# Optimization experiments

Hardware: AMD Instinct MI355X
Metric: run time of the kernel (lower is better)

The kernel has to match this reference:

```python
import jax, jax.numpy as jnp
import numpy as np

B, L, D, H, O = 512, 256, 256, 128, 256  # batch, max_len, input_dim, hidden_dim, output_dim


def setup_inputs() -> dict:
    key = jax.random.key(0)
    ks = jax.random.split(key, 16)
    s = 0.1
    n = jax.random.normal
    return {
        "sequences": n(ks[0], (B, L, D), jnp.float32),
        "seqlens": jax.random.randint(ks[1], (B,), 1, L + 1, jnp.int32),
        # forward-direction GRU params (PyTorch layout: gates [r, z, n] stacked)
        "Wih_f": s * n(ks[2], (3 * H, D), jnp.float32),
        "Whh_f": s * n(ks[3], (3 * H, H), jnp.float32),
        "bih_f": s * n(ks[4], (3 * H,), jnp.float32),
        "bhh_f": s * n(ks[5], (3 * H,), jnp.float32),
        # backward-direction GRU params
        "Wih_b": s * n(ks[6], (3 * H, D), jnp.float32),
        "Whh_b": s * n(ks[7], (3 * H, H), jnp.float32),
        "bih_b": s * n(ks[8], (3 * H,), jnp.float32),
        "bhh_b": s * n(ks[9], (3 * H,), jnp.float32),
        # attention MLP + context vector
        "W_mlp": s * n(ks[10], (O, 2 * H), jnp.float32),
        "b_mlp": s * n(ks[11], (O,), jnp.float32),
        "ctx": s * n(ks[12], (O,), jnp.float32),
    }


def _gru(xs, mask, Wih, Whh, bih, bhh, reverse):
    """Masked GRU scan. xs: [L,B,D], mask: [L,B,1]. Returns hidden states [L,B,H]."""
    def step(h, inp):
        x_t, m_t = inp
        gx = x_t @ Wih.T + bih          # [B, 3H]
        gh = h @ Whh.T + bhh            # [B, 3H]
        xr, xz, xn = jnp.split(gx, 3, axis=-1)
        hr, hz, hn = jnp.split(gh, 3, axis=-1)
        r = jax.nn.sigmoid(xr + hr)
        z = jax.nn.sigmoid(xz + hz)
        cand = jnp.tanh(xn + r * hn)
        h_new = (1.0 - z) * cand + z * h
        h = jnp.where(m_t, h_new, h)    # hold state on padding steps
        return h, h

    h0 = jnp.zeros((xs.shape[1], Whh.shape[1]), xs.dtype)
    _, hs = jax.lax.scan(step, h0, (xs, mask), reverse=reverse)
    return hs


def reference(sequences, seqlens, Wih_f, Whh_f, bih_f, bhh_f, Wih_b, Whh_b, bih_b, bhh_b, W_mlp, b_mlp, ctx):
    mask = jnp.arange(L)[None, :] < seqlens[:, None]      # [B, L] valid-token mask
    xs = sequences.transpose(1, 0, 2)                      # [L, B, D]
    m = mask.T[:, :, None]                                 # [L, B, 1]
    hf = _gru(xs, m, Wih_f, Whh_f, bih_f, bhh_f, False)    # forward direction
    hb = _gru(xs, m, Wih_b, Whh_b, bih_b, bhh_b, True)     # backward direction
    rnn_out = jnp.concatenate([hf, hb], axis=-1).transpose(1, 0, 2)  # [B, L, 2H]
    mlp_out = jnp.tanh(rnn_out @ W_mlp.T + b_mlp)          # [B, L, O]
    scores = jnp.einsum('blo,o->bl', mlp_out, ctx)         # [B, L]
    neg = jnp.finfo(scores.dtype).min
    w = jax.nn.softmax(jnp.where(mask, scores, neg), axis=1)  # per-sequence softmax over valid positions
    return jnp.einsum('bl,blh->bh', w, rnn_out)            # [B, 2H] attention-pooled embedding
```

## Files before the change

kernel.cpp:

```cpp
#include <hip/hip_runtime.h>
#include <hip/hip_bf16.h>
#include <cstdint>
#include <cstddef>

#define BATCH 512
#define SEQL 256
#define DIN 256
#define HID 128
#define OUTD 256
#define G3 384
#define TCH 64
#define NCH 4
#define NBS 16
#define NGRPS (BATCH/NBS)
#define MTOT (BATCH*SEQL)
#define MCH  (BATCH*TCH)
#define HSPAD 136
#define NGXT 3072

typedef __attribute__((ext_vector_type(8))) short short8v;
typedef __attribute__((ext_vector_type(4))) float float4v;

__device__ __forceinline__ unsigned short f2bf_u(float x) {
  union { float f; uint32_t u; } v; v.f = x;
  uint32_t r = v.u + 0x7FFFu + ((v.u >> 16) & 1u);
  return (unsigned short)(r >> 16);
}
__device__ __forceinline__ float bfu2f(unsigned short u) {
  union { uint32_t u; float f; } v; v.u = ((uint32_t)u) << 16; return v.f;
}
__device__ __forceinline__ float fast_tanh(float x) {
  float e2 = __expf(-2.0f * x);
  return (1.0f - e2) / (1.0f + e2);
}

__global__ __launch_bounds__(256) void prep_split(
    const float* __restrict__ Wm, unsigned short* __restrict__ mhi, unsigned short* __restrict__ mlo,
    const float* __restrict__ Wf, unsigned short* __restrict__ fhi, unsigned short* __restrict__ flo,
    const float* __restrict__ Wb, unsigned short* __restrict__ bhi, unsigned short* __restrict__ blo)
{
  int gid = blockIdx.x * 256 + threadIdx.x;
  const float* src; unsigned short* hi; unsigned short* lo; int off;
  if (gid < 16384)      { src = Wm; hi = mhi; lo = mlo; off = gid * 4; }
  else if (gid < 40960) { src = Wf; hi = fhi; lo = flo; off = (gid - 16384) * 4; }
  else                  { src = Wb; hi = bhi; lo = blo; off = (gid - 40960) * 4; }
  float4 w4 = *(const float4*)&src[off];
  ushort4 h4, l4;
  h4.x = f2bf_u(w4.x); l4.x = f2bf_u(w4.x - bfu2f(h4.x));
  h4.y = f2bf_u(w4.y); l4.y = f2bf_u(w4.y - bfu2f(h4.y));
  h4.z = f2bf_u(w4.z); l4.z = f2bf_u(w4.z - bfu2f(h4.z));
  h4.w = f2bf_u(w4.w); l4.w = f2bf_u(w4.w - bfu2f(h4.w));
  *(ushort4*)&hi[off] = h4;
  *(ushort4*)&lo[off] = l4;
}

__device__ __forceinline__ void gx_tile(
    int tid, int m0, int yy,
    const float* __restrict__ X,
    const unsigned short* __restrict__ WhiF, const unsigned short* __restrict__ WloF,
    const unsigned short* __restrict__ WhiB, const unsigned short* __restrict__ WloB,
    const float* __restrict__ bf, const float* __restrict__ bb,
    unsigned short* __restrict__ bufF, unsigned short* __restrict__ bufB, int cF, int cB,
    unsigned short* Abf, unsigned short* Bhi, unsigned short* Blo)
{
  const unsigned short* Whi; const unsigned short* Wlo;
  const float* bias; unsigned short* buf; int c;
  if (yy < 6) { Whi = WhiF; Wlo = WloF; bias = bf; buf = bufF; c = cF; }
  else        { yy -= 6; Whi = WhiB; Wlo = WloB; bias = bb; buf = bufB; c = cB; }
  const int n0 = yy * 64;

  const int l  = tid & 63;
  const int w  = tid >> 6;
  const int fr = l & 15;
  const int fk = (l >> 4) * 8;

  float4v acc[2][4];
#pragma unroll
  for (int a = 0; a < 2; ++a)
#pragma unroll
    for (int nb = 0; nb < 4; ++nb) acc[a][nb] = (float4v)0.0f;

  for (int k0 = 0; k0 < DIN; k0 += 32) {
#pragma unroll
    for (int j = 0; j < 4; ++j) {
      int row = (tid >> 3) + j * 32;
      int kq  = (tid & 7) * 4;
      int r   = m0 + row;
      int b_  = r >> 6, tt = r & 63;
      int xrow = b_ * SEQL + c * TCH + tt;
      float4 x4 = *(const float4*)&X[(size_t)xrow * DIN + k0 + kq];
      ushort4 h4 = {f2bf_u(x4.x), f2bf_u(x4.y), f2bf_u(x4.z), f2bf_u(x4.w)};
      *(ushort4*)&Abf[row * 40 + kq] = h4;
    }
    {
      int half = tid & 1;
      int cc   = tid >> 1;
      int col  = cc >> 1;
      int seg  = (cc & 1) * 16;
      const unsigned short* srcw = (half ? Wlo : Whi) + (size_t)(n0 + col) * DIN + k0 + seg;
      unsigned short* dst = (half ? Blo : Bhi) + col * 40 + seg;
      *(short8v*)dst       = *(const short8v*)srcw;
      *(short8v*)(dst + 8) = *(const short8v*)(srcw + 8);
    }
    __syncthreads();

    short8v ah[2], bh[4], blv[4];
#pragma unroll
    for (int a = 0; a < 2; ++a)
      ah[a] = *(const short8v*)&Abf[(w * 32 + a * 16 + fr) * 40 + fk];
#pragma unroll
    for (int nb = 0; nb < 4; ++nb) {
      bh[nb]  = *(const short8v*)&Bhi[(nb * 16 + fr) * 40 + fk];
      blv[nb] = *(const short8v*)&Blo[(nb * 16 + fr) * 40 + fk];
    }
#pragma unroll
    for (int a = 0; a < 2; ++a)
#pragma unroll
      for (int nb = 0; nb < 4; ++nb) {
        acc[a][nb] = __builtin_amdgcn_mfma_f32_16x16x32_bf16(ah[a], bh[nb],  acc[a][nb], 0, 0, 0);
        acc[a][nb] = __builtin_amdgcn_mfma_f32_16x16x32_bf16(ah[a], blv[nb], acc[a][nb], 0, 0, 0);
      }
    __syncthreads();
  }

#pragma unroll
  for (int a = 0; a < 2; ++a)
#pragma unroll
    for (int nb = 0; nb < 4; ++nb) {
      int gate = n0 + nb * 16 + fr;
      float bv_ = bias[gate];
#pragma unroll
      for (int reg = 0; reg < 4; ++reg) {
        int r = m0 + w * 32 + a * 16 + (l >> 4) * 4 + reg;
        buf[(size_t)r * G3 + gate] = f2bf_u(acc[a][nb][reg] + bv_);
      }
    }
}

template<int P>
__device__ __forceinline__ void gru_step(
    unsigned short (*hsbuf)[NBS * HSPAD], int col, int rq, int hidx,
    const short8v (&Bh)[3][4], const short8v (&Bl)[3][4], const float (&bias_)[3],
    const float (&G)[3][4], float (&hold)[4], const int (&len_)[4], int t,
    __hip_bfloat16* (&rp)[4], int drp)
{
  const unsigned short* rd = &hsbuf[P][col * HSPAD + rq * 8];
  short8v ah[4];
#pragma unroll
  for (int ks = 0; ks < 4; ++ks)
    ah[ks] = *(const short8v*)(rd + ks * 32);

  float4v a0 = (float4v){bias_[0] + G[0][0], bias_[0] + G[0][1], bias_[0] + G[0][2], bias_[0] + G[0][3]};
  float4v a1 = (float4v){bias_[1] + G[1][0], bias_[1] + G[1][1], bias_[1] + G[1][2], bias_[1] + G[1][3]};
  float4v a2 = (float4v){bias_[2], bias_[2], bias_[2], bias_[2]};
  float4v l0 = (float4v)0.0f, l1 = (float4v)0.0f, l2 = (float4v)0.0f;
#pragma unroll
  for (int ks = 0; ks < 4; ++ks) {
    a0 = __builtin_amdgcn_mfma_f32_16x16x32_bf16(ah[ks], Bh[0][ks], a0, 0, 0, 0);
    l0 = __builtin_amdgcn_mfma_f32_16x16x32_bf16(ah[ks], Bl[0][ks], l0, 0, 0, 0);
    a1 = __builtin_amdgcn_mfma_f32_16x16x32_bf16(ah[ks], Bh[1][ks], a1, 0, 0, 0);
    l1 = __builtin_amdgcn_mfma_f32_16x16x32_bf16(ah[ks], Bl[1][ks], l1, 0, 0, 0);
    a2 = __builtin_amdgcn_mfma_f32_16x16x32_bf16(ah[ks], Bh[2][ks], a2, 0, 0, 0);
    l2 = __builtin_amdgcn_mfma_f32_16x16x32_bf16(ah[ks], Bl[2][ks], l2, 0, 0, 0);
  }
  a0 += l0; a1 += l1; a2 += l2;

  unsigned short* wr = &hsbuf[P ^ 1][rq * 4 * HSPAD + hidx];
#pragma unroll
  for (int reg = 0; reg < 4; ++reg) {
    float gr = a0[reg], gz = a1[reg], gn = a2[reg], xn = G[2][reg];
    float r = 1.0f / (1.0f + __expf(-gr));
    float z = 1.0f / (1.0f + __expf(-gz));
    float e2 = __expf(-2.0f * (xn + r * gn));
    float cand = (1.0f - e2) / (1.0f + e2);
    float hv = cand + z * (hold[reg] - cand);
    bool act = (t < len_[reg]);
    hv = act ? hv : hold[reg];
    hold[reg] = hv;
    wr[reg * HSPAD] = f2bf_u(hv);
    if (act) *rp[reg] = __float2bfloat16(hv);
    rp[reg] += drp;
  }
  asm volatile("s_waitcnt lgkmcnt(0)" ::: "memory");
  __builtin_amdgcn_s_barrier();
  __builtin_amdgcn_sched_barrier(0);
}

__device__ __forceinline__ void scan_block(
    int sb, int tid,
    const int* __restrict__ seqlens,
    const float* __restrict__ Whh_f, const float* __restrict__ Whh_b,
    const float* __restrict__ bhh_f, const float* __restrict__ bhh_b,
    const unsigned short* __restrict__ bufF, const unsigned short* __restrict__ bufB,
    float* __restrict__ hstate, __hip_bfloat16* __restrict__ rnn, int ci,
    unsigned short (*hsbuf)[NBS * HSPAD])
{
  const int fwd = (sb < NGRPS) ? 1 : 0;
  const int grp = fwd ? sb : (sb - NGRPS);
  const int b0  = grp * NBS;
  const int w   = tid >> 6;
  const int l   = tid & 63;
  const int col = l & 15;
  const int rq  = l >> 4;
  const int hidx = w * 16 + col;
  const float* Whh = fwd ? Whh_f : Whh_b;
  const float* bhh = fwd ? bhh_f : bhh_b;
  const unsigned short* buf = fwd ? bufF : bufB;
  const int c = fwd ? ci : (NCH - 1 - ci);

  __builtin_amdgcn_s_setprio(1);

  short8v Bh[3][4], Bl[3][4];
  float bias_[3];
#pragma unroll
  for (int j = 0; j < 3; ++j) {
    const int g = j * HID + hidx;
    bias_[j] = bhh[g];
#pragma unroll
    for (int ks = 0; ks < 4; ++ks) {
      const float* p = Whh + (size_t)g * HID + ks * 32 + rq * 8;
      float4 x0 = *(const float4*)p;
      float4 x1 = *(const float4*)(p + 4);
      float v[8] = {x0.x, x0.y, x0.z, x0.w, x1.x, x1.y, x1.z, x1.w};
      short8v hi8, lo8;
#pragma unroll
      for (int e = 0; e < 8; ++e) {
        unsigned short h = f2bf_u(v[e]);
        hi8[e] = (short)h;
        lo8[e] = (short)f2bf_u(v[e] - bfu2f(h));
      }
      Bh[j][ks] = hi8; Bl[j][ks] = lo8;
    }
  }

  int len_[4];
#pragma unroll
  for (int reg = 0; reg < 4; ++reg) len_[reg] = seqlens[b0 + rq * 4 + reg];
  int gmax = 0;
  for (int nb = 0; nb < NBS; ++nb) gmax = max(gmax, seqlens[b0 + nb]);

  float* hst = hstate + ((size_t)((fwd ? 0 : 1) * NGRPS + grp)) * (NBS * HID);
  float hold[4];
#pragma unroll
  for (int reg = 0; reg < 4; ++reg) {
    int nb = rq * 4 + reg;
    hold[reg] = (ci == 0) ? 0.0f : hst[nb * HID + hidx];
    hsbuf[0][nb * HSPAD + hidx] = f2bf_u(hold[reg]);
  }
  __syncthreads();

  int nsteps = gmax - c * TCH;
  nsteps = (nsteps > TCH) ? TCH : nsteps;

  const int tcb  = c * TCH;
  const int dofs = fwd ? 0 : HID;

  if (nsteps == TCH) {
    const int tt0 = fwd ? 0 : (TCH - 1);
    const int dt  = fwd ? 1 : -1;
    const int dgp = fwd ? G3 : -G3;
    const int drp = fwd ? OUTD : -OUTD;

    const unsigned short* gp[4];
    __hip_bfloat16* rp[4];
#pragma unroll
    for (int reg = 0; reg < 4; ++reg) {
      gp[reg] = buf + (size_t)((b0 + rq * 4 + reg) * TCH + tt0) * G3 + hidx;
      rp[reg] = rnn + (size_t)((b0 + rq * 4 + reg) * SEQL + tcb + tt0) * OUTD + dofs + hidx;
    }

    float GA[3][4], GB[3][4];
    auto LOADGX = [&](float (&G)[3][4]) {
#pragma unroll
      for (int reg = 0; reg < 4; ++reg) {
        G[0][reg] = bfu2f(gp[reg][0]);
        G[1][reg] = bfu2f(gp[reg][HID]);
        G[2][reg] = bfu2f(gp[reg][2 * HID]);
        gp[reg] += dgp;
      }
    };
    LOADGX(GA);
    LOADGX(GB);

    int t = tcb + tt0;
#pragma unroll 1
    for (int it = 0; it < TCH / 2; ++it) {
      gru_step<0>(hsbuf, col, rq, hidx, Bh, Bl, bias_, GA, hold, len_, t, rp, drp);
      t += dt;
      LOADGX(GA);
      gru_step<1>(hsbuf, col, rq, hidx, Bh, Bl, bias_, GB, hold, len_, t, rp, drp);
      t += dt;
      LOADGX(GB);
    }
  } else if (nsteps > 0) {
    float gxc[3][4], gxn[3][4];
    {
      int tt0 = fwd ? 0 : (nsteps - 1);
#pragma unroll
      for (int j = 0; j < 3; ++j)
#pragma unroll
        for (int reg = 0; reg < 4; ++reg)
          gxc[j][reg] = bfu2f(buf[(size_t)((b0 + rq * 4 + reg) * TCH + tt0) * G3 + j * HID + hidx]);
    }

    int cur = 0;
    for (int ss = 0; ss < nsteps; ++ss) {
      const int tt = fwd ? ss : (nsteps - 1 - ss);
      const int t  = tcb + tt;

      short8v ah[4];
#pragma unroll
      for (int ks = 0; ks < 4; ++ks)
        ah[ks] = *(const short8v*)&hsbuf[cur][col * HSPAD + ks * 32 + rq * 8];

      {
        int ssn = (ss + 1 < nsteps) ? (ss + 1) : ss;
        int ttn = fwd ? ssn : (nsteps - 1 - ssn);
#pragma unroll
        for (int j = 0; j < 3; ++j)
#pragma unroll
          for (int reg = 0; reg < 4; ++reg)
            gxn[j][reg] = bfu2f(buf[(size_t)((b0 + rq * 4 + reg) * TCH + ttn) * G3 + j * HID + hidx]);
      }

      float4v acc[3], accl[3];
#pragma unroll
      for (int j = 0; j < 3; ++j) {
        acc[j]  = (float4v){bias_[j], bias_[j], bias_[j], bias_[j]};
        accl[j] = (float4v)0.0f;
      }
#pragma unroll
      for (int ks = 0; ks < 4; ++ks) {
#pragma unroll
        for (int j = 0; j < 3; ++j) {
          acc[j]  = __builtin_amdgcn_mfma_f32_16x16x32_bf16(ah[ks], Bh[j][ks], acc[j],  0, 0, 0);
          accl[j] = __builtin_amdgcn_mfma_f32_16x16x32_bf16(ah[ks], Bl[j][ks], accl[j], 0, 0, 0);
        }
      }
#pragma unroll
      for (int j = 0; j < 3; ++j) acc[j] += accl[j];

#pragma unroll
      for (int reg = 0; reg < 4; ++reg) {
        int nb = rq * 4 + reg;
        float gr = acc[0][reg] + gxc[0][reg];
        float gz = acc[1][reg] + gxc[1][reg];
        float gn = acc[2][reg];
        float xn = gxc[2][reg];
        float r = 1.0f / (1.0f + __expf(-gr));
        float z = 1.0f / (1.0f + __expf(-gz));
        float e2 = __expf(-2.0f * (xn + r * gn));
        float cand = (1.0f - e2) / (1.0f + e2);
        float hv = (1.0f - z) * cand + z * hold[reg];
        bool act = (t < len_[reg]);
        hv = act ? hv : hold[reg];
        hold[reg] = hv;
        hsbuf[cur ^ 1][nb * HSPAD + hidx] = f2bf_u(hv);
        if (act)
          rnn[(size_t)((b0 + nb) * SEQL + t) * OUTD + dofs + hidx] = __float2bfloat16(hv);
      }
      asm volatile("s_waitcnt lgkmcnt(0)" ::: "memory");
      __builtin_amdgcn_s_barrier();
      __builtin_amdgcn_sched_barrier(0);
      cur ^= 1;

#pragma unroll
      for (int j = 0; j < 3; ++j)
#pragma unroll
        for (int reg = 0; reg < 4; ++reg) gxc[j][reg] = gxn[j][reg];
    }
  }

  __builtin_amdgcn_s_setprio(0);

#pragma unroll
  for (int reg = 0; reg < 4; ++reg)
    hst[(rq * 4 + reg) * HID + hidx] = hold[reg];
}

__device__ __forceinline__ void mlp64_tile(
    int tid, int m0, int nh,
    const __hip_bfloat16* __restrict__ rnn,
    const unsigned short* __restrict__ Whi, const unsigned short* __restrict__ Wlo,
    const float* __restrict__ bmlp, const float* __restrict__ ctx,
    float* __restrict__ scoresH,
    unsigned short* Abf, unsigned short* BhiS, unsigned short* BloS)
{
  const int l  = tid & 63;
  const int w  = tid >> 6;
  const int fr = l & 15;
  const int fk = (l >> 4) * 8;

  float bl_[8], cl_[8];
#pragma unroll
  for (int nt = 0; nt < 8; ++nt) {
    bl_[nt] = bmlp[nh * 128 + nt * 16 + fr];
    cl_[nt] = ctx[nh * 128 + nt * 16 + fr];
  }

  float4v acc[8];
#pragma unroll
  for (int nt = 0; nt < 8; ++nt) acc[nt] = (float4v)0.0f;

  for (int k0 = 0; k0 < OUTD; k0 += 32) {
    {
      int row = tid >> 2;
      int kq  = (tid & 3) * 8;
      *(short8v*)&Abf[row * 40 + kq] =
          *(const short8v*)((const short*)rnn + (size_t)(m0 + row) * OUTD + k0 + kq);
    }
#pragma unroll
    for (int j = 0; j < 2; ++j) {
      int cid  = tid * 2 + j;
      int half = cid >> 8;
      int cc   = cid & 255;
      int colx = cc >> 1;
      int seg  = (cc & 1) * 16;
      const unsigned short* srcw = (half ? Wlo : Whi) + (size_t)(nh * 128 + colx) * OUTD + k0 + seg;
      unsigned short* dst = (half ? BloS : BhiS) + colx * 40 + seg;
      *(short8v*)dst       = *(const short8v*)srcw;
      *(short8v*)(dst + 8) = *(const short8v*)(srcw + 8);
    }
    __syncthreads();

    short8v a = *(const short8v*)&Abf[(w * 16 + fr) * 40 + fk];
#pragma unroll
    for (int nt = 0; nt < 8; ++nt) {
      short8v bh = *(const short8v*)&BhiS[(nt * 16 + fr) * 40 + fk];
      short8v bv = *(const short8v*)&BloS[(nt * 16 + fr) * 40 + fk];
      acc[nt] = __builtin_amdgcn_mfma_f32_16x16x32_bf16(a, bh, acc[nt], 0, 0, 0);
      acc[nt] = __builtin_amdgcn_mfma_f32_16x16x32_bf16(a, bv, acc[nt], 0, 0, 0);
    }
    __syncthreads();
  }

  float p[4] = {0.f, 0.f, 0.f, 0.f};
#pragma unroll
  for (int nt = 0; nt < 8; ++nt) {
    float bv_ = bl_[nt], cv = cl_[nt];
#pragma unroll
    for (int reg = 0; reg < 4; ++reg)
      p[reg] += fast_tanh(acc[nt][reg] + bv_) * cv;
  }
#pragma unroll
  for (int off = 1; off < 16; off <<= 1)
#pragma unroll
    for (int reg = 0; reg < 4; ++reg) p[reg] += __shfl_xor(p[reg], off, 64);
  if (fr == 0) {
#pragma unroll
    for (int reg = 0; reg < 4; ++reg)
      scoresH[(size_t)nh * MTOT + m0 + w * 16 + (l >> 4) * 4 + reg] = p[reg];
  }
}

__global__ __launch_bounds__(256) void gx_kernel(
    const float* __restrict__ X,
    const unsigned short* __restrict__ WhiF, const unsigned short* __restrict__ WloF,
    const unsigned short* __restrict__ WhiB, const unsigned short* __restrict__ WloB,
    const float* __restrict__ bf, const float* __restrict__ bb,
    unsigned short* __restrict__ bufF, unsigned short* __restrict__ bufB, int cF, int cB)
{
  __shared__ unsigned short Abf[128 * 40];
  __shared__ unsigned short Bhi[64 * 40];
  __shared__ unsigned short Blo[64 * 40];
  gx_tile(threadIdx.x, blockIdx.x * 128, blockIdx.y, X, WhiF, WloF, WhiB, WloB,
          bf, bb, bufF, bufB, cF, cB, Abf, Bhi, Blo);
}

__global__ __launch_bounds__(512, 2) void scan_kernel(
    const int* __restrict__ seqlens,
    const float* __restrict__ Whh_f, const float* __restrict__ Whh_b,
    const float* __restrict__ bhh_f, const float* __restrict__ bhh_b,
    const unsigned short* __restrict__ bufF, const unsigned short* __restrict__ bufB,
    float* __restrict__ hstate, __hip_bfloat16* __restrict__ rnn, int ci)
{
  __shared__ unsigned short hsbuf[2][NBS * HSPAD];
  scan_block(blockIdx.x, threadIdx.x, seqlens, Whh_f, Whh_b, bhh_f, bhh_b,
             bufF, bufB, hstate, rnn, ci, hsbuf);
}

__global__ __launch_bounds__(512, 2) void fused_kernel(
    const int* __restrict__ seqlens,
    const float* __restrict__ Whh_f, const float* __restrict__ Whh_b,
    const float* __restrict__ bhh_f, const float* __restrict__ bhh_b,
    const float* __restrict__ X,
    const unsigned short* __restrict__ WhiF, const unsigned short* __restrict__ WloF,
    const unsigned short* __restrict__ WhiB, const unsigned short* __restrict__ WloB,
    const float* __restrict__ bf, const float* __restrict__ bb,
    const unsigned short* __restrict__ rdF, const unsigned short* __restrict__ rdB,
    unsigned short* __restrict__ wrF, unsigned short* __restrict__ wrB,
    float* __restrict__ hstate, __hip_bfloat16* __restrict__ rnn, int ci)
{
  __shared__ unsigned short hsbuf[2][NBS * HSPAD];
  __shared__ unsigned short AbfS[2][128 * 40];
  __shared__ unsigned short BhiS[2][64 * 40];
  __shared__ unsigned short BloS[2][64 * 40];

  if (blockIdx.x < 2 * NGRPS) {
    scan_block(blockIdx.x, threadIdx.x, seqlens, Whh_f, Whh_b, bhh_f, bhh_b,
               rdF, rdB, hstate, rnn, ci, hsbuf);
  } else {
    const int gb   = blockIdx.x - 2 * NGRPS;
    const int half = threadIdx.x >> 8;
    const int htid = threadIdx.x & 255;
    const int t0   = gb * 2 + half;
    const int m0   = (t0 & 255) * 128;
    const int yy   = t0 >> 8;
    gx_tile(htid, m0, yy, X, WhiF, WloF, WhiB, WloB, bf, bb,
            wrF, wrB, ci + 1, NCH - 2 - ci, AbfS[half], BhiS[half], BloS[half]);
  }
}

union ShFinal {
  unsigned short hs[2][NBS * HSPAD];
  struct { unsigned short A[2][64 * 40]; unsigned short Bh[2][128 * 40]; unsigned short Bl[2][128 * 40]; } m;
};
__global__ __launch_bounds__(512, 2) void fused_final(
    const int* __restrict__ seqlens,
    const float* __restrict__ Whh_f, const float* __restrict__ Whh_b,
    const float* __restrict__ bhh_f, const float* __restrict__ bhh_b,
    const unsigned short* __restrict__ rdF, const unsigned short* __restrict__ rdB,
    float* __restrict__ hstate, __hip_bfloat16* __restrict__ rnn,
    const unsigned short* __restrict__ mhi, const unsigned short* __restrict__ mlo,
    const float* __restrict__ bmlp, const float* __restrict__ ctx,
    float* __restrict__ scoresH)
{
  __shared__ ShFinal sh;
  if (blockIdx.x < 2 * NGRPS) {
    scan_block(blockIdx.x, threadIdx.x, seqlens, Whh_f, Whh_b, bhh_f, bhh_b,
               rdF, rdB, hstate, rnn, NCH - 1, sh.hs);
  } else {
    const int gb   = blockIdx.x - 2 * NGRPS;
    const int half = threadIdx.x >> 8;
    const int htid = threadIdx.x & 255;
    const int body = gb * 2 + half;
    const int nh   = body & 1;
    const int tile = body >> 1;
    const int b    = tile >> 1;
    const int t0   = 64 + (tile & 1) * 64;
    const int m0   = b * SEQL + t0;
    mlp64_tile(htid, m0, nh, rnn, mhi, mlo, bmlp, ctx, scoresH,
               sh.m.A[half], sh.m.Bh[half], sh.m.Bl[half]);
  }
}

__global__ __launch_bounds__(256) void mlp_score(
    const __hip_bfloat16* __restrict__ rnn,
    const unsigned short* __restrict__ Whi, const unsigned short* __restrict__ Wlo,
    const float* __restrict__ bmlp, const float* __restrict__ ctx,
    float* __restrict__ scoresH)
{
  __shared__ unsigned short Abf[128 * 40];
  __shared__ unsigned short BhiS[128 * 40];
  __shared__ unsigned short BloS[128 * 40];

  const int tid = threadIdx.x;
  const int m0  = blockIdx.x * 128;
  const int nh  = blockIdx.y;
  const int l   = tid & 63;
  const int w   = tid >> 6;
  const int fr  = l & 15;
  const int fk  = (l >> 4) * 8;

  float bl_[8], cl_[8];
#pragma unroll
  for (int nt = 0; nt < 8; ++nt) {
    bl_[nt] = bmlp[nh * 128 + nt * 16 + fr];
    cl_[nt] = ctx[nh * 128 + nt * 16 + fr];
  }

  float4v acc[2][8];
#pragma unroll
  for (int a = 0; a < 2; ++a)
#pragma unroll
    for (int nt = 0; nt < 8; ++nt) acc[a][nt] = (float4v)0.0f;

  for (int k0 = 0; k0 < OUTD; k0 += 32) {
    {
      int row = tid >> 1;
      int kq  = (tid & 1) * 16;
      const short* src = (const short*)rnn + (size_t)(m0 + row) * OUTD + k0 + kq;
      *(short8v*)&Abf[row * 40 + kq]     = *(const short8v*)src;
      *(short8v*)&Abf[row * 40 + kq + 8] = *(const short8v*)(src + 8);
    }
#pragma unroll
    for (int j = 0; j < 2; ++j) {
      int cid  = tid * 2 + j;
      int half = cid >> 8;
      int cc   = cid & 255;
      int colx = cc >> 1;
      int seg  = (cc & 1) * 16;
      const unsigned short* srcw = (half ? Wlo : Whi) + (size_t)(nh * 128 + colx) * OUTD + k0 + seg;
      unsigned short* dst = (half ? BloS : BhiS) + colx * 40 + seg;
      *(short8v*)dst       = *(const short8v*)srcw;
      *(short8v*)(dst + 8) = *(const short8v*)(srcw + 8);
    }
    __syncthreads();

    short8v ah0 = *(const short8v*)&Abf[(w * 32 + fr) * 40 + fk];
    short8v ah1 = *(const short8v*)&Abf[(w * 32 + 16 + fr) * 40 + fk];
#pragma unroll
    for (int nt = 0; nt < 8; ++nt) {
      short8v bh = *(const short8v*)&BhiS[(nt * 16 + fr) * 40 + fk];
      short8v bv = *(const short8v*)&BloS[(nt * 16 + fr) * 40 + fk];
      acc[0][nt] = __builtin_amdgcn_mfma_f32_16x16x32_bf16(ah0, bh, acc[0][nt], 0, 0, 0);
      acc[0][nt] = __builtin_amdgcn_mfma_f32_16x16x32_bf16(ah0, bv, acc[0][nt], 0, 0, 0);
      acc[1][nt] = __builtin_amdgcn_mfma_f32_16x16x32_bf16(ah1, bh, acc[1][nt], 0, 0, 0);
      acc[1][nt] = __builtin_amdgcn_mfma_f32_16x16x32_bf16(ah1, bv, acc[1][nt], 0, 0, 0);
    }
    __syncthreads();
  }

#pragma unroll
  for (int a = 0; a < 2; ++a) {
    float p[4] = {0.f, 0.f, 0.f, 0.f};
#pragma unroll
    for (int nt = 0; nt < 8; ++nt) {
      float bv_ = bl_[nt], cv = cl_[nt];
#pragma unroll
      for (int reg = 0; reg < 4; ++reg)
        p[reg] += fast_tanh(acc[a][nt][reg] + bv_) * cv;
    }
#pragma unroll
    for (int off = 1; off < 16; off <<= 1)
#pragma unroll
      for (int reg = 0; reg < 4; ++reg) p[reg] += __shfl_xor(p[reg], off, 64);
    if (fr == 0) {
#pragma unroll
      for (int reg = 0; reg < 4; ++reg)
        scoresH[(size_t)nh * MTOT + m0 + w * 32 + a * 16 + (l >> 4) * 4 + reg] = p[reg];
    }
  }
}

__global__ __launch_bounds__(256) void mlp_score_rest(
    const __hip_bfloat16* __restrict__ rnn,
    const unsigned short* __restrict__ Whi, const unsigned short* __restrict__ Wlo,
    const float* __restrict__ bmlp, const float* __restrict__ ctx,
    float* __restrict__ scoresH)
{
  __shared__ unsigned short Abf[128 * 40];
  __shared__ unsigned short BhiS[128 * 40];
  __shared__ unsigned short BloS[128 * 40];

  const int tid = threadIdx.x;
  const int b   = blockIdx.x;
  const int nh  = blockIdx.y;
  const int l   = tid & 63;
  const int w   = tid >> 6;
  const int fr  = l & 15;
  const int fk  = (l >> 4) * 8;

  float bl_[8], cl_[8];
#pragma unroll
  for (int nt = 0; nt < 8; ++nt) {
    bl_[nt] = bmlp[nh * 128 + nt * 16 + fr];
    cl_[nt] = ctx[nh * 128 + nt * 16 + fr];
  }

  float4v acc[2][8];
#pragma unroll
  for (int a = 0; a < 2; ++a)
#pragma unroll
    for (int nt = 0; nt < 8; ++nt) acc[a][nt] = (float4v)0.0f;

  for (int k0 = 0; k0 < OUTD; k0 += 32) {
    {
      int row = tid >> 1;
      int kq  = (tid & 1) * 16;
      int t   = (row < 64) ? row : (row + 128);
      const short* src = (const short*)rnn + (size_t)(b * SEQL + t) * OUTD + k0 + kq;
      *(short8v*)&Abf[row * 40 + kq]     = *(const short8v*)src;
      *(short8v*)&Abf[row * 40 + kq + 8] = *(const short8v*)(src + 8);
    }
#pragma unroll
    for (int j = 0; j < 2; ++j) {
      int cid  = tid * 2 + j;
      int half = cid >> 8;
      int cc   = cid & 255;
      int colx = cc >> 1;
      int seg  = (cc & 1) * 16;
      const unsigned short* srcw = (half ? Wlo : Whi) + (size_t)(nh * 128 + colx) * OUTD + k0 + seg;
      unsigned short* dst = (half ? BloS : BhiS) + colx * 40 + seg;
      *(short8v*)dst       = *(const short8v*)srcw;
      *(short8v*)(dst + 8) = *(const short8v*)(srcw + 8);
    }
    __syncthreads();

    short8v ah0 = *(const short8v*)&Abf[(w * 32 + fr) * 40 + fk];
    short8v ah1 = *(const short8v*)&Abf[(w * 32 + 16 + fr) * 40 + fk];
#pragma unroll
    for (int nt = 0; nt < 8; ++nt) {
      short8v bh = *(const short8v*)&BhiS[(nt * 16 + fr) * 40 + fk];
      short8v bv = *(const short8v*)&BloS[(nt * 16 + fr) * 40 + fk];
      acc[0][nt] = __builtin_amdgcn_mfma_f32_16x16x32_bf16(ah0, bh, acc[0][nt], 0, 0, 0);
      acc[0][nt] = __builtin_amdgcn_mfma_f32_16x16x32_bf16(ah0, bv, acc[0][nt], 0, 0, 0);
      acc[1][nt] = __builtin_amdgcn_mfma_f32_16x16x32_bf16(ah1, bh, acc[1][nt], 0, 0, 0);
      acc[1][nt] = __builtin_amdgcn_mfma_f32_16x16x32_bf16(ah1, bv, acc[1][nt], 0, 0, 0);
    }
    __syncthreads();
  }

#pragma unroll
  for (int a = 0; a < 2; ++a) {
    float p[4] = {0.f, 0.f, 0.f, 0.f};
#pragma unroll
    for (int nt = 0; nt < 8; ++nt) {
      float bv_ = bl_[nt], cv = cl_[nt];
#pragma unroll
      for (int reg = 0; reg < 4; ++reg)
        p[reg] += fast_tanh(acc[a][nt][reg] + bv_) * cv;
    }
#pragma unroll
    for (int off = 1; off < 16; off <<= 1)
#pragma unroll
      for (int reg = 0; reg < 4; ++reg) p[reg] += __shfl_xor(p[reg], off, 64);
    if (fr == 0) {
#pragma unroll
      for (int reg = 0; reg < 4; ++reg) {
        int rr = w * 32 + a * 16 + (l >> 4) * 4 + reg;
        int t  = (rr < 64) ? rr : (rr + 128);
        scoresH[(size_t)nh * MTOT + b * SEQL + t] = p[reg];
      }
    }
  }
}

__global__ __launch_bounds__(256) void softmax_pool(
    const int* __restrict__ seqlens,
    const float* __restrict__ scoresH,
    const __hip_bfloat16* __restrict__ rnn,
    float* __restrict__ out)
{
  const int b = blockIdx.x;
  const int len = seqlens[b];
  const int tid = threadIdx.x;
  __shared__ float sm[SEQL];
  __shared__ float red[8];

  float s = (tid < len)
      ? (scoresH[b * SEQL + tid] + scoresH[(size_t)MTOT + b * SEQL + tid])
      : -3.4e38f;
  float wm = s;
#pragma unroll
  for (int off = 32; off > 0; off >>= 1) wm = fmaxf(wm, __shfl_xor(wm, off, 64));
  if ((tid & 63) == 0) red[tid >> 6] = wm;
  __syncthreads();
  float bm = fmaxf(fmaxf(red[0], red[1]), fmaxf(red[2], red[3]));

  float e = (tid < len) ? expf(s - bm) : 0.0f;
  sm[tid] = e;
  float sum = e;
#pragma unroll
  for (int off = 32; off > 0; off >>= 1) sum += __shfl_xor(sum, off, 64);
  if ((tid & 63) == 0) red[4 + (tid >> 6)] = sum;
  __syncthreads();
  float inv = 1.0f / (red[4] + red[5] + red[6] + red[7]);

  float acc = 0.0f;
  for (int l = 0; l < len; ++l)
    acc += sm[l] * __bfloat162float(rnn[(size_t)(b * SEQL + l) * OUTD + tid]);
  out[b * OUTD + tid] = acc * inv;
}

extern "C" void kernel_launch(void* const* d_in, const int* in_sizes, int n_in,
                              void* d_out, int out_size, void* d_ws, size_t ws_size,
                              hipStream_t stream) {
  const float* seq    = (const float*)d_in[0];
  const int*   lens   = (const int*)d_in[1];
  const float* Wih_f  = (const float*)d_in[2];
  const float* Whh_f  = (const float*)d_in[3];
  const float* bih_f  = (const float*)d_in[4];
  const float* bhh_f  = (const float*)d_in[5];
  const float* Wih_b  = (const float*)d_in[6];
  const float* Whh_b  = (const float*)d_in[7];
  const float* bih_b  = (const float*)d_in[8];
  const float* bhh_b  = (const float*)d_in[9];
  const float* Wmlp   = (const float*)d_in[10];
  const float* bmlp   = (const float*)d_in[11];
  const float* ctx    = (const float*)d_in[12];
  float* out = (float*)d_out;

  const size_t BUFSZ = (size_t)MCH * G3;
  const size_t needOverlap =
      4 * BUFSZ * 2 + (size_t)MTOT * OUTD * 2 + 2 * (size_t)MTOT * 4 +
      2 * BATCH * HID * 4 + 2 * (size_t)OUTD * OUTD * 2 + 4 * (size_t)G3 * DIN * 2;
  const bool overlap = (ws_size >= needOverlap);

  unsigned short* buf0F = (unsigned short*)d_ws;
  unsigned short* buf0B = buf0F + BUFSZ;
  unsigned short* buf1F = overlap ? (buf0B + BUFSZ) : buf0F;
  unsigned short* buf1B = overlap ? (buf1F + BUFSZ) : buf0B;
  unsigned short* tail  = overlap ? (buf1B + BUFSZ) : (buf0B + BUFSZ);

  __hip_bfloat16* rnn  = (__hip_bfloat16*)tail;
  float* scoresH = (float*)((unsigned short*)rnn + (size_t)MTOT * OUTD);
  float* hstate  = scoresH + 2 * (size_t)MTOT;
  unsigned short* mhi = (unsigned short*)(hstate + 2 * BATCH * HID);
  unsigned short* mlo = mhi + OUTD * OUTD;
  unsigned short* fhi = mlo + OUTD * OUTD;
  unsigned short* flo = fhi + G3 * DIN;
  unsigned short* bhi2 = flo + G3 * DIN;
  unsigned short* blo2 = bhi2 + G3 * DIN;

  prep_split<<<dim3(256), 256, 0, stream>>>(Wmlp, mhi, mlo, Wih_f, fhi, flo, Wih_b, bhi2, blo2);

  if (overlap) {
    unsigned short* bp[2][2] = {{buf0F, buf0B}, {buf1F, buf1B}};
    gx_kernel<<<dim3(256, 12), 256, 0, stream>>>(seq, fhi, flo, bhi2, blo2, bih_f, bih_b,
                                                 bp[0][0], bp[0][1], 0, NCH - 1);
    for (int k = 0; k < NCH - 1; ++k) {
      fused_kernel<<<dim3(2 * NGRPS + NGXT / 2), 512, 0, stream>>>(
          lens, Whh_f, Whh_b, bhh_f, bhh_b,
          seq, fhi, flo, bhi2, blo2, bih_f, bih_b,
          bp[k & 1][0], bp[k & 1][1], bp[(k + 1) & 1][0], bp[(k + 1) & 1][1],
          hstate, rnn, k);
    }
    fused_final<<<dim3(2 * NGRPS + 1024), 512, 0, stream>>>(
        lens, Whh_f, Whh_b, bhh_f, bhh_b,
        bp[(NCH - 1) & 1][0], bp[(NCH - 1) & 1][1], hstate, rnn,
        mhi, mlo, bmlp, ctx, scoresH);
    mlp_score_rest<<<dim3(512, 2), 256, 0, stream>>>(rnn, mhi, mlo, bmlp, ctx, scoresH);
  } else {
    for (int ci = 0; ci < NCH; ++ci) {
      gx_kernel<<<dim3(256, 12), 256, 0, stream>>>(seq, fhi, flo, bhi2, blo2, bih_f, bih_b,
                                                   buf0F, buf0B, ci, NCH - 1 - ci);
      scan_kernel<<<dim3(2 * NGRPS), 512, 0, stream>>>(
          lens, Whh_f, Whh_b, bhh_f, bhh_b, buf0F, buf0B, hstate, rnn, ci);
    }
    mlp_score<<<dim3(MTOT / 128, 2), 256, 0, stream>>>(rnn, mhi, mlo, bmlp, ctx, scoresH);
  }

  softmax_pool<<<dim3(BATCH), 256, 0, stream>>>(lens, scoresH, rnn, out);
}
```

Before: 525.3 us.

## Fuse remaining MLP scoring with softmax pooling and deepen gx prefetch in scan

The separate mlp_score_rest and softmax_pool launches are merged into one per-batch tail_kernel. It computes the MLP scores for the remaining timesteps of both output halves, combines them with the precomputed middle scores in shared memory, and then does the masked softmax and pooling. This removes one launch and the global round-trip of those scores, but halves the grid from 1024 to 512 blocks. The GRU scan loop also now prefetches the input-gate values two steps ahead as raw bf16 in a 4-deep rotation, to hide global load latency behind the recurrent step.

Result: slower. 627.1 us (+19.4%).

```diff
diff --git a/kernel.cpp b/kernel.cpp
--- a/kernel.cpp
+++ b/kernel.cpp
@@ -34,6 +34,8 @@
   return (1.0f - e2) / (1.0f + e2);
 }
 
+struct GxB { unsigned short v[3][4]; };
+
 __global__ __launch_bounds__(256) void prep_split(
     const float* __restrict__ Wm, unsigned short* __restrict__ mhi, unsigned short* __restrict__ mlo,
     const float* __restrict__ Wf, unsigned short* __restrict__ fhi, unsigned short* __restrict__ flo,
@@ -138,20 +140,32 @@
 }
 
 template<int P>
-__device__ __forceinline__ void gru_step(
+__device__ __forceinline__ void gru_step2(
     unsigned short (*hsbuf)[NBS * HSPAD], int col, int rq, int hidx,
     const short8v (&Bh)[3][4], const short8v (&Bl)[3][4], const float (&bias_)[3],
-    const float (&G)[3][4], float (&hold)[4], const int (&len_)[4], int t,
+    const GxB& Gc, GxB& Gl,
+    const unsigned short* (&gp)[4], int dgp,
+    float (&hold)[4], const int (&len_)[4], int t,
     __hip_bfloat16* (&rp)[4], int drp)
 {
+#pragma unroll
+  for (int reg = 0; reg < 4; ++reg) {
+    Gl.v[0][reg] = gp[reg][0];
+    Gl.v[1][reg] = gp[reg][HID];
+    Gl.v[2][reg] = gp[reg][2 * HID];
+    gp[reg] += dgp;
+  }
+
   const unsigned short* rd = &hsbuf[P][col * HSPAD + rq * 8];
   short8v ah[4];
 #pragma unroll
   for (int ks = 0; ks < 4; ++ks)
     ah[ks] = *(const short8v*)(rd + ks * 32);
 
-  float4v a0 = (float4v){bias_[0] + G[0][0], bias_[0] + G[0][1], bias_[0] + G[0][2], bias_[0] + G[0][3]};
-  float4v a1 = (float4v){bias_[1] + G[1][0], bias_[1] + G[1][1], bias_[1] + G[1][2], bias_[1] + G[1][3]};
+  float4v a0 = (float4v){bias_[0] + bfu2f(Gc.v[0][0]), bias_[0] + bfu2f(Gc.v[0][1]),
+                         bias_[0] + bfu2f(Gc.v[0][2]), bias_[0] + bfu2f(Gc.v[0][3])};
+  float4v a1 = (float4v){bias_[1] + bfu2f(Gc.v[1][0]), bias_[1] + bfu2f(Gc.v[1][1]),
+                         bias_[1] + bfu2f(Gc.v[1][2]), bias_[1] + bfu2f(Gc.v[1][3])};
   float4v a2 = (float4v){bias_[2], bias_[2], bias_[2], bias_[2]};
   float4v l0 = (float4v)0.0f, l1 = (float4v)0.0f, l2 = (float4v)0.0f;
 #pragma unroll
@@ -168,7 +182,8 @@
   unsigned short* wr = &hsbuf[P ^ 1][rq * 4 * HSPAD + hidx];
 #pragma unroll
   for (int reg = 0; reg < 4; ++reg) {
-    float gr = a0[reg], gz = a1[reg], gn = a2[reg], xn = G[2][reg];
+    float gr = a0[reg], gz = a1[reg], gn = a2[reg];
+    float xn = bfu2f(Gc.v[2][reg]);
     float r = 1.0f / (1.0f + __expf(-gr));
     float z = 1.0f / (1.0f + __expf(-gz));
     float e2 = __expf(-2.0f * (xn + r * gn));
@@ -269,28 +284,25 @@
       rp[reg] = rnn + (size_t)((b0 + rq * 4 + reg) * SEQL + tcb + tt0) * OUTD + dofs + hidx;
     }
 
-    float GA[3][4], GB[3][4];
-    auto LOADGX = [&](float (&G)[3][4]) {
-#pragma unroll
-      for (int reg = 0; reg < 4; ++reg) {
-        G[0][reg] = bfu2f(gp[reg][0]);
-        G[1][reg] = bfu2f(gp[reg][HID]);
-        G[2][reg] = bfu2f(gp[reg][2 * HID]);
-        gp[reg] += dgp;
-      }
-    };
-    LOADGX(GA);
-    LOADGX(GB);
+    GxB g0, g1, g2, g3;
+#pragma unroll
+    for (int reg = 0; reg < 4; ++reg) {
+      g0.v[0][reg] = gp[reg][0]; g0.v[1][reg] = gp[reg][HID]; g0.v[2][reg] = gp[reg][2 * HID];
+      gp[reg] += dgp;
+    }
+#pragma unroll
+    for (int reg = 0; reg < 4; ++reg) {
+      g1.v[0][reg] = gp[reg][0]; g1.v[1][reg] = gp[reg][HID]; g1.v[2][reg] = gp[reg][2 * HID];
+      gp[reg] += dgp;
+    }
 
     int t = tcb + tt0;
 #pragma unroll 1
-    for (int it = 0; it < TCH / 2; ++it) {
-      gru_step<0>(hsbuf, col, rq, hidx, Bh, Bl, bias_, GA, hold, len_, t, rp, drp);
-      t += dt;
-      LOADGX(GA);
-      gru_step<1>(hsbuf, col, rq, hidx, Bh, Bl, bias_, GB, hold, len_, t, rp, drp);
-      t += dt;
-      LOADGX(GB);
+    for (int it = 0; it < TCH / 4; ++it) {
+      gru_step2<0>(hsbuf, col, rq, hidx, Bh, Bl, bias_, g0, g2, gp, dgp, hold, len_, t, rp, drp); t += dt;
+      gru_step2<1>(hsbuf, col, rq, hidx, Bh, Bl, bias_, g1, g3, gp, dgp, hold, len_, t, rp, drp); t += dt;
+      gru_step2<0>(hsbuf, col, rq, hidx, Bh, Bl, bias_, g2, g0, gp, dgp, hold, len_, t, rp, drp); t += dt;
+      gru_step2<1>(hsbuf, col, rq, hidx, Bh, Bl, bias_, g3, g1, gp, dgp, hold, len_, t, rp, drp); t += dt;
     }
   } else if (nsteps > 0) {
     float gxc[3][4], gxn[3][4];
@@ -544,6 +556,137 @@
   }
 }
 
+__global__ __launch_bounds__(256) void tail_kernel(
+    const int* __restrict__ seqlens,
+    const __hip_bfloat16* __restrict__ rnn,
+    const unsigned short* __restrict__ Whi, const unsigned short* __restrict__ Wlo,
+    const float* __restrict__ bmlp, const float* __restrict__ ctx,
+    const float* __restrict__ scoresH,
+    float* __restrict__ out)
+{
+  __shared__ unsigned short Abf[128 * 40];
+  __shared__ unsigned short BhiS[128 * 40];
+  __shared__ unsigned short BloS[128 * 40];
+  __shared__ float sm[SEQL];
+  __shared__ float red[8];
+
+  const int tid = threadIdx.x;
+  const int b   = blockIdx.x;
+  const int len = seqlens[b];
+  const int l   = tid & 63;
+  const int w   = tid >> 6;
+  const int fr  = l & 15;
+  const int fk  = (l >> 4) * 8;
+
+  float pfull[2][4] = {{0.f, 0.f, 0.f, 0.f}, {0.f, 0.f, 0.f, 0.f}};
+
+  for (int nh = 0; nh < 2; ++nh) {
+    float bl_[8], cl_[8];
+#pragma unroll
+    for (int nt = 0; nt < 8; ++nt) {
+      bl_[nt] = bmlp[nh * 128 + nt * 16 + fr];
+      cl_[nt] = ctx[nh * 128 + nt * 16 + fr];
+    }
+
+    float4v acc[2][8];
+#pragma unroll
+    for (int a = 0; a < 2; ++a)
+#pragma unroll
+      for (int nt = 0; nt < 8; ++nt) acc[a][nt] = (float4v)0.0f;
+
+    for (int k0 = 0; k0 < OUTD; k0 += 32) {
+      {
+        int row = tid >> 1;
+        int kq  = (tid & 1) * 16;
+        int t   = (row < 64) ? row : (row + 128);
+        const short* src = (const short*)rnn + (size_t)(b * SEQL + t) * OUTD + k0 + kq;
+        *(short8v*)&Abf[row * 40 + kq]     = *(const short8v*)src;
+        *(short8v*)&Abf[row * 40 + kq + 8] = *(const short8v*)(src + 8);
+      }
+#pragma unroll
+      for (int j = 0; j < 2; ++j) {
+        int cid  = tid * 2 + j;
+        int half = cid >> 8;
+        int cc   = cid & 255;
+        int colx = cc >> 1;
+        int seg  = (cc & 1) * 16;
+        const unsigned short* srcw = (half ? Wlo : Whi) + (size_t)(nh * 128 + colx) * OUTD + k0 + seg;
+        unsigned short* dst = (half ? BloS : BhiS) + colx * 40 + seg;
+        *(short8v*)dst       = *(const short8v*)srcw;
+        *(short8v*)(dst + 8) = *(const short8v*)(srcw + 8);
+      }
+      __syncthreads();
+
+      short8v ah0 = *(const short8v*)&Abf[(w * 32 + fr) * 40 + fk];
+      short8v ah1 = *(const short8v*)&Abf[(w * 32 + 16 + fr) * 40 + fk];
+#pragma unroll
+      for (int nt = 0; nt < 8; ++nt) {
+        short8v bh = *(const short8v*)&BhiS[(nt * 16 + fr) * 40 + fk];
+        short8v bv = *(const short8v*)&BloS[(nt * 16 + fr) * 40 + fk];
+        acc[0][nt] = __builtin_amdgcn_mfma_f32_16x16x32_bf16(ah0, bh, acc[0][nt], 0, 0, 0);
+        acc[0][nt] = __builtin_amdgcn_mfma_f32_16x16x32_bf16(ah0, bv, acc[0][nt], 0, 0, 0);
+        acc[1][nt] = __builtin_amdgcn_mfma_f32_16x16x32_bf16(ah1, bh, acc[1][nt], 0, 0, 0);
+        acc[1][nt] = __builtin_amdgcn_mfma_f32_16x16x32_bf16(ah1, bv, acc[1][nt], 0, 0, 0);
+      }
+      __syncthreads();
+    }
+
+#pragma unroll
+    for (int a = 0; a < 2; ++a)
+#pragma unroll
+      for (int nt = 0; nt < 8; ++nt) {
+        float bv_ = bl_[nt], cv = cl_[nt];
+#pragma unroll
+        for (int reg = 0; reg < 4; ++reg)
+          pfull[a][reg] += fast_tanh(acc[a][nt][reg] + bv_) * cv;
+      }
+  }
+
+#pragma unroll
+  for (int a = 0; a < 2; ++a) {
+#pragma unroll
+    for (int off = 1; off < 16; off <<= 1)
+#pragma unroll
+      for (int reg = 0; reg < 4; ++reg) pfull[a][reg] += __shfl_xor(pfull[a][reg], off, 64);
+  }
+  if (fr == 0) {
+#pragma unroll
+    for (int a = 0; a < 2; ++a)
+#pragma unroll
+      for (int reg = 0; reg < 4; ++reg) {
+        int rr = w * 32 + a * 16 + (l >> 4) * 4 + reg;
+        int t  = (rr < 64) ? rr : (rr + 128);
+        sm[t] = pfull[a][reg];
+      }
+  }
+  if (tid < 128)
+    sm[64 + tid] = scoresH[b * SEQL + 64 + tid] + scoresH[(size_t)MTOT + b * SEQL + 64 + tid];
+  __syncthreads();
+
+  float s = (tid < len) ? sm[tid] : -3.4e38f;
+  float wm = s;
+#pragma unroll
+  for (int off = 32; off > 0; off >>= 1) wm = fmaxf(wm, __shfl_xor(wm, off, 64));
+  if ((tid & 63) == 0) red[tid >> 6] = wm;
+  __syncthreads();
+  float bm = fmaxf(fmaxf(red[0], red[1]), fmaxf(red[2], red[3]));
+
+  float e = (tid < len) ? __expf(s - bm) : 0.0f;
+  __syncthreads();
+  sm[tid] = e;
+  float sum = e;
+#pragma unroll
+  for (int off = 32; off > 0; off >>= 1) sum += __shfl_xor(sum, off, 64);
+  if ((tid & 63) == 0) red[4 + (tid >> 6)] = sum;
+  __syncthreads();
+  float inv = 1.0f / (red[4] + red[5] + red[6] + red[7]);
+
+  float acc = 0.0f;
+  for (int l2 = 0; l2 < len; ++l2)
+    acc += sm[l2] * __bfloat162float(rnn[(size_t)(b * SEQL + l2) * OUTD + tid]);
+  out[b * OUTD + tid] = acc * inv;
+}
+
 __global__ __launch_bounds__(256) void mlp_score(
     const __hip_bfloat16* __restrict__ rnn,
     const unsigned short* __restrict__ Whi, const unsigned short* __restrict__ Wlo,
@@ -629,99 +772,6 @@
 #pragma unroll
       for (int reg = 0; reg < 4; ++reg)
         scoresH[(size_t)nh * MTOT + m0 + w * 32 + a * 16 + (l >> 4) * 4 + reg] = p[reg];
-    }
-  }
-}
-
-__global__ __launch_bounds__(256) void mlp_score_rest(
-    const __hip_bfloat16* __restrict__ rnn,
-    const unsigned short* __restrict__ Whi, const unsigned short* __restrict__ Wlo,
-    const float* __restrict__ bmlp, const float* __restrict__ ctx,
-    float* __restrict__ scoresH)
-{
-  __shared__ unsigned short Abf[128 * 40];
-  __shared__ unsigned short BhiS[128 * 40];
-  __shared__ unsigned short BloS[128 * 40];
-
-  const int tid = threadIdx.x;
-  const int b   = blockIdx.x;
-  const int nh  = blockIdx.y;
-  const int l   = tid & 63;
-  const int w   = tid >> 6;
-  const int fr  = l & 15;
-  const int fk  = (l >> 4) * 8;
-
-  float bl_[8], cl_[8];
-#pragma unroll
-  for (int nt = 0; nt < 8; ++nt) {
-    bl_[nt] = bmlp[nh * 128 + nt * 16 + fr];
-    cl_[nt] = ctx[nh * 128 + nt * 16 + fr];
-  }
-
-  float4v acc[2][8];
-#pragma unroll
-  for (int a = 0; a < 2; ++a)
-#pragma unroll
-    for (int nt = 0; nt < 8; ++nt) acc[a][nt] = (float4v)0.0f;
-
-  for (int k0 = 0; k0 < OUTD; k0 += 32) {
-    {
-      int row = tid >> 1;
-      int kq  = (tid & 1) * 16;
-      int t   = (row < 64) ? row : (row + 128);
-      const short* src = (const short*)rnn + (size_t)(b * SEQL + t) * OUTD + k0 + kq;
-      *(short8v*)&Abf[row * 40 + kq]     = *(const short8v*)src;
-      *(short8v*)&Abf[row * 40 + kq + 8] = *(const short8v*)(src + 8);
-    }
-#pragma unroll
-    for (int j = 0; j < 2; ++j) {
-      int cid  = tid * 2 + j;
-      int half = cid >> 8;
-      int cc   = cid & 255;
-      int colx = cc >> 1;
-      int seg  = (cc & 1) * 16;
-      const unsigned short* srcw = (half ? Wlo : Whi) + (size_t)(nh * 128 + colx) * OUTD + k0 + seg;
-      unsigned short* dst = (half ? BloS : BhiS) + colx * 40 + seg;
-      *(short8v*)dst       = *(const short8v*)srcw;
-      *(short8v*)(dst + 8) = *(const short8v*)(srcw + 8);
-    }
-    __syncthreads();
-
-    short8v ah0 = *(const short8v*)&Abf[(w * 32 + fr) * 40 + fk];
-    short8v ah1 = *(const short8v*)&Abf[(w * 32 + 16 + fr) * 40 + fk];
-#pragma unroll
-    for (int nt = 0; nt < 8; ++nt) {
-      short8v bh = *(const short8v*)&BhiS[(nt * 16 + fr) * 40 + fk];
-      short8v bv = *(const short8v*)&BloS[(nt * 16 + fr) * 40 + fk];
-      acc[0][nt] = __builtin_amdgcn_mfma_f32_16x16x32_bf16(ah0, bh, acc[0][nt], 0, 0, 0);
-      acc[0][nt] = __builtin_amdgcn_mfma_f32_16x16x32_bf16(ah0, bv, acc[0][nt], 0, 0, 0);
-      acc[1][nt] = __builtin_amdgcn_mfma_f32_16x16x32_bf16(ah1, bh, acc[1][nt], 0, 0, 0);
-      acc[1][nt] = __builtin_amdgcn_mfma_f32_16x16x32_bf16(ah1, bv, acc[1][nt], 0, 0, 0);
-    }
-    __syncthreads();
-  }
-
-#pragma unroll
-  for (int a = 0; a < 2; ++a) {
-    float p[4] = {0.f, 0.f, 0.f, 0.f};
-#pragma unroll
-    for (int nt = 0; nt < 8; ++nt) {
-      float bv_ = bl_[nt], cv = cl_[nt];
-#pragma unroll
-      for (int reg = 0; reg < 4; ++reg)
-        p[reg] += fast_tanh(acc[a][nt][reg] + bv_) * cv;
-    }
-#pragma unroll
-    for (int off = 1; off < 16; off <<= 1)
-#pragma unroll
-      for (int reg = 0; reg < 4; ++reg) p[reg] += __shfl_xor(p[reg], off, 64);
-    if (fr == 0) {
-#pragma unroll
-      for (int reg = 0; reg < 4; ++reg) {
-        int rr = w * 32 + a * 16 + (l >> 4) * 4 + reg;
-        int t  = (rr < 64) ? rr : (rr + 128);
-        scoresH[(size_t)nh * MTOT + b * SEQL + t] = p[reg];
-      }
     }
   }
 }
@@ -820,7 +870,7 @@
         lens, Whh_f, Whh_b, bhh_f, bhh_b,
         bp[(NCH - 1) & 1][0], bp[(NCH - 1) & 1][1], hstate, rnn,
         mhi, mlo, bmlp, ctx, scoresH);
-    mlp_score_rest<<<dim3(512, 2), 256, 0, stream>>>(rnn, mhi, mlo, bmlp, ctx, scoresH);
+    tail_kernel<<<dim3(BATCH), 256, 0, stream>>>(lens, rnn, mhi, mlo, bmlp, ctx, scoresH, out);
   } else {
     for (int ci = 0; ci < NCH; ++ci) {
       gx_kernel<<<dim3(256, 12), 256, 0, stream>>>(seq, fhi, flo, bhi2, blo2, bih_f, bih_b,
@@ -829,7 +879,6 @@
           lens, Whh_f, Whh_b, bhh_f, bhh_b, buf0F, buf0B, hstate, rnn, ci);
     }
     mlp_score<<<dim3(MTOT / 128, 2), 256, 0, stream>>>(rnn, mhi, mlo, bmlp, ctx, scoresH);
-  }
-
-  softmax_pool<<<dim3(BATCH), 256, 0, stream>>>(lens, scoresH, rnn, out);
-}
+    softmax_pool<<<dim3(BATCH), 256, 0, stream>>>(lens, scoresH, rnn, out);
+  }
+}
```
